# Optimization experiments

Hardware: AMD Instinct MI355X
Metric: run time of the kernel (lower is better)

Reference implementation:

```python
import jax, jax.numpy as jnp
from jax import lax
import numpy as np

INF = 1e10


def _fps_indices(xyz, npoint, start):
    """Farthest point sampling. xyz:(B,N,3), start:(B,) int32 -> (B,npoint) indices."""
    B, N, _ = xyz.shape

    def step(carry, _):
        distance, farthest = carry  # (B,N), (B,)
        # gather current centroid: (B,1,3)
        centroid = xyz[jnp.arange(B), farthest][:, None, :]
        dist = jnp.sum((xyz - centroid) ** 2, axis=-1)  # (B,N)
        distance = jnp.minimum(distance, dist)  # torch where(dist<distance, dist, distance)
        new_farthest = jnp.argmax(distance, axis=-1)
        return (distance, new_farthest), farthest

    init_dist = jnp.full((B, N), INF, dtype=xyz.dtype)
    (_, _), centroids = lax.scan(step, (init_dist, start), None, length=npoint)
    return centroids.T  # (B, npoint)


def setup_inputs() -> dict:
    key = jax.random.key(0)
    B, N = 16, 131072
    xyz = jax.random.normal(key, (B, N, 3), dtype=jnp.float32)
    return {"xyz": xyz, "npoint": 1024}


def reference(xyz, npoint):
    B, N, _ = xyz.shape
    # torch code picks a random starting index per batch; use a fixed jax PRNG
    start = jax.random.randint(jax.random.fold_in(jax.random.key(0), 1), (B,), 0, N)
    idx = _fps_indices(xyz, npoint, start)  # (B, npoint) int
    new_xyz = xyz[jnp.arange(B)[:, None], idx]  # (B, npoint, 3)
    return new_xyz, idx
```

## Files before the change

kernel.cpp:

```cpp
#include <hip/hip_runtime.h>
#include <stdint.h>

#define NB   16
#define WPB  16
#define NTHR 512
#define PPT  16

__device__ __forceinline__ void tf2x32(uint32_t k0, uint32_t k1,
                                       uint32_t x0, uint32_t x1,
                                       uint32_t &y0, uint32_t &y1) {
  uint32_t ks2 = k0 ^ k1 ^ 0x1BD11BDAu;
  uint32_t v0 = x0 + k0, v1 = x1 + k1;
#define TFR(r) { v0 += v1; v1 = (v1 << (r)) | (v1 >> (32 - (r))); v1 ^= v0; }
  TFR(13) TFR(15) TFR(26) TFR(6)   v0 += k1;  v1 += ks2 + 1u;
  TFR(17) TFR(29) TFR(16) TFR(24)  v0 += ks2; v1 += k0 + 2u;
  TFR(13) TFR(15) TFR(26) TFR(6)   v0 += k0;  v1 += k1 + 3u;
  TFR(17) TFR(29) TFR(16) TFR(24)  v0 += k1;  v1 += ks2 + 4u;
  TFR(13) TFR(15) TFR(26) TFR(6)   v0 += ks2; v1 += k0 + 5u;
#undef TFR
  y0 = v0; y1 = v1;
}

__global__ __launch_bounds__(NTHR, 4)
void FPSampler_42099269435595_kernel(const float* __restrict__ xyz,
                                     const int* __restrict__ npoint_ptr,
                                     float* __restrict__ out,
                                     unsigned long long* __restrict__ slots,
                                     int N) {
  const int blk  = blockIdx.x;
  const int b    = blk >> 4;
  const int w    = blk & (WPB - 1);
  const int tid  = threadIdx.x;
  const int wave = tid >> 6;
  const int lane = tid & 63;
  const int npoint = npoint_ptr[0];

  const float* __restrict__ xb = xyz + (size_t)b * N * 3;
  const int pts_per_wg = N / WPB;
  const int p0 = w * pts_per_wg + tid;

  float px[PPT], py[PPT], pz[PPT], dist[PPT];
#pragma unroll
  for (int k = 0; k < PPT; ++k) {
    size_t p = (size_t)(p0 + k * NTHR);
    px[k] = xb[3 * p + 0];
    py[k] = xb[3 * p + 1];
    pz[k] = xb[3 * p + 2];
    dist[k] = 1e10f;
  }

  uint32_t fk0, fk1, s0, s1, r0, r1;
  tf2x32(0u, 0u, 0u, 1u, fk0, fk1);
  tf2x32(fk0, fk1, 0u, 1u, s0, s1);
  tf2x32(s0, s1, 0u, (uint32_t)b, r0, r1);
  uint32_t far = (r0 ^ r1) & 0x1FFFFu;

  __shared__ unsigned long long lds_red[NTHR / 64];
  __shared__ unsigned long long lds_win;

  float* out_xyz = out;
  float* out_idx = out + (size_t)NB * npoint * 3;

  for (int i = 0; i < npoint; ++i) {
    float cx = xb[3 * (size_t)far + 0];
    float cy = xb[3 * (size_t)far + 1];
    float cz = xb[3 * (size_t)far + 2];
    if (w == 0 && tid == 0) {
      size_t o = (size_t)b * npoint + i;
      out_xyz[3 * o + 0] = cx;
      out_xyz[3 * o + 1] = cy;
      out_xyz[3 * o + 2] = cz;
      out_idx[o] = (float)far;
    }
    if (i == npoint - 1) break;

    float best = -1.0f;
    uint32_t bidx = 0;
#pragma unroll
    for (int k = 0; k < PPT; ++k) {
#pragma clang fp contract(off)
      float dx = px[k] - cx, dy = py[k] - cy, dz = pz[k] - cz;
      float d = (dx * dx + dy * dy) + dz * dz;
      float nd = fminf(dist[k], d);
      dist[k] = nd;
      if (nd > best) { best = nd; bidx = (uint32_t)(p0 + k * NTHR); }
    }

    unsigned long long pk =
        ((unsigned long long)(uint32_t)(i + 1) << 51) |
        ((unsigned long long)__float_as_uint(best) << 19) |
        (unsigned long long)(0x7FFFFu - bidx);

#pragma unroll
    for (int off = 32; off >= 1; off >>= 1) {
      unsigned long long o = __shfl_xor(pk, off);
      if (o > pk) pk = o;
    }
    if (lane == 0) lds_red[wave] = pk;
    __syncthreads();

    unsigned long long* myslot = &slots[((size_t)(i & 1) * NB + b) * WPB];
    if (tid == 0) {
      unsigned long long m = lds_red[0];
#pragma unroll
      for (int q = 1; q < NTHR / 64; ++q)
        if (lds_red[q] > m) m = lds_red[q];
      __hip_atomic_store(&myslot[w], m, __ATOMIC_RELAXED,
                         __HIP_MEMORY_SCOPE_AGENT);
    }
    if (wave == 0) {
      unsigned long long v = 0;
      if (lane < WPB) {
        const uint32_t tag = (uint32_t)(i + 1);
        do {
          v = __hip_atomic_load(&myslot[lane], __ATOMIC_RELAXED,
                                __HIP_MEMORY_SCOPE_AGENT);
        } while ((uint32_t)(v >> 51) != tag);
      }
#pragma unroll
      for (int off = 8; off >= 1; off >>= 1) {
        unsigned long long o = __shfl_xor(v, off);
        if (o > v) v = o;
      }
      if (lane == 0) lds_win = v;
    }
    __syncthreads();
    far = 0x7FFFFu - (uint32_t)(lds_win & 0x7FFFFu);
  }
}

extern "C" void kernel_launch(void* const* d_in, const int* in_sizes, int n_in,
                              void* d_out, int out_size, void* d_ws, size_t ws_size,
                              hipStream_t stream) {
  const float* xyz = (const float*)d_in[0];
  const int* npoint = (const int*)d_in[1];
  int N = in_sizes[0] / (NB * 3);

  hipMemsetAsync(d_ws, 0, (size_t)2 * NB * WPB * sizeof(unsigned long long),
                 stream);
  FPSampler_42099269435595_kernel<<<NB * WPB, NTHR, 0, stream>>>(
      xyz, npoint, (float*)d_out, (unsigned long long*)d_ws, N);
}
```

Baseline: 2.506 ms.

## Carry winner coordinates through cross-block exchange to avoid global centroid reload

Each thread tracks the coordinates of its best point, and each wave picks them out with ballot and shuffle. Every workgroup publishes its key plus x/y/z as four tagged 64-bit words in the slot array. Wave 0 of every block then polls all 64 words in parallel and takes the winning centroid directly, so the dependent global load of the next centroid at the start of each iteration goes away. The block-level reduction moves from a serial loop in one thread to a shuffle across wave 0. This costs more atomic stores and polling traffic per iteration and lowers the launch-bounds occupancy hint to 2.

```diff
diff --git a/kernel.cpp b/kernel.cpp
--- a/kernel.cpp
+++ b/kernel.cpp
@@ -1,10 +1,11 @@
 #include <hip/hip_runtime.h>
 #include <stdint.h>
 
-#define NB   16
-#define WPB  16
-#define NTHR 512
-#define PPT  16
+#define NB    16
+#define WPB   16
+#define NTHR  512
+#define NWAVE (NTHR / 64)
+#define PPT   16
 
 __device__ __forceinline__ void tf2x32(uint32_t k0, uint32_t k1,
                                        uint32_t x0, uint32_t x1,
@@ -21,7 +22,8 @@
   y0 = v0; y1 = v1;
 }
 
-__global__ __launch_bounds__(NTHR, 4)
+
+__global__ __launch_bounds__(NTHR, 2)
 void FPSampler_42099269435595_kernel(const float* __restrict__ xyz,
                                      const int* __restrict__ npoint_ptr,
                                      float* __restrict__ out,
@@ -36,8 +38,7 @@
   const int npoint = npoint_ptr[0];
 
   const float* __restrict__ xb = xyz + (size_t)b * N * 3;
-  const int pts_per_wg = N / WPB;
-  const int p0 = w * pts_per_wg + tid;
+  const int p0 = w * (N / WPB) + tid;
 
   float px[PPT], py[PPT], pz[PPT], dist[PPT];
 #pragma unroll
@@ -48,6 +49,10 @@
     pz[k] = xb[3 * p + 2];
     dist[k] = 1e10f;
   }
+#pragma unroll
+  for (int k = 0; k < PPT; ++k) {
+    asm volatile("" : "+v"(px[k]), "+v"(py[k]), "+v"(pz[k]));
+  }
 
   uint32_t fk0, fk1, s0, s1, r0, r1;
   tf2x32(0u, 0u, 0u, 1u, fk0, fk1);
@@ -55,16 +60,19 @@
   tf2x32(s0, s1, 0u, (uint32_t)b, r0, r1);
   uint32_t far = (r0 ^ r1) & 0x1FFFFu;
 
-  __shared__ unsigned long long lds_red[NTHR / 64];
-  __shared__ unsigned long long lds_win;
+  float cx = xb[3 * (size_t)far + 0];
+  float cy = xb[3 * (size_t)far + 1];
+  float cz = xb[3 * (size_t)far + 2];
+
+  __shared__ unsigned long long lds_key[NWAVE];
+  __shared__ float lds_x[NWAVE], lds_y[NWAVE], lds_z[NWAVE];
+  __shared__ unsigned int lds_bfar;
+  __shared__ float lds_bcx, lds_bcy, lds_bcz;
 
   float* out_xyz = out;
   float* out_idx = out + (size_t)NB * npoint * 3;
 
   for (int i = 0; i < npoint; ++i) {
-    float cx = xb[3 * (size_t)far + 0];
-    float cy = xb[3 * (size_t)far + 1];
-    float cz = xb[3 * (size_t)far + 2];
     if (w == 0 && tid == 0) {
       size_t o = (size_t)b * npoint + i;
       out_xyz[3 * o + 0] = cx;
@@ -74,7 +82,7 @@
     }
     if (i == npoint - 1) break;
 
-    float best = -1.0f;
+    float best = -1.0f, bx = 0.f, by = 0.f, bz = 0.f;
     uint32_t bidx = 0;
 #pragma unroll
     for (int k = 0; k < PPT; ++k) {
@@ -83,49 +91,92 @@
       float d = (dx * dx + dy * dy) + dz * dz;
       float nd = fminf(dist[k], d);
       dist[k] = nd;
-      if (nd > best) { best = nd; bidx = (uint32_t)(p0 + k * NTHR); }
+      if (nd > best) {
+        best = nd; bidx = (uint32_t)(p0 + k * NTHR);
+        bx = px[k]; by = py[k]; bz = pz[k];
+      }
     }
 
-    unsigned long long pk =
-        ((unsigned long long)(uint32_t)(i + 1) << 51) |
+    unsigned long long mykey =
         ((unsigned long long)__float_as_uint(best) << 19) |
         (unsigned long long)(0x7FFFFu - bidx);
-
+    unsigned long long pk = mykey;
 #pragma unroll
     for (int off = 32; off >= 1; off >>= 1) {
       unsigned long long o = __shfl_xor(pk, off);
       if (o > pk) pk = o;
     }
-    if (lane == 0) lds_red[wave] = pk;
+    unsigned long long bal = __ballot(mykey == pk);
+    int wl = __ffsll(bal) - 1;
+    float wx = __shfl(bx, wl), wy = __shfl(by, wl), wz = __shfl(bz, wl);
+    if (lane == 0) {
+      lds_key[wave] = pk;
+      lds_x[wave] = wx; lds_y[wave] = wy; lds_z[wave] = wz;
+    }
     __syncthreads();
 
-    unsigned long long* myslot = &slots[((size_t)(i & 1) * NB + b) * WPB];
-    if (tid == 0) {
-      unsigned long long m = lds_red[0];
+    unsigned long long* base =
+        slots + (size_t)(((i & 1) * NB + b)) * (WPB * 4);
+    const uint32_t tag = (uint32_t)(i + 1);
+
+    if (wave == 0) {
+      unsigned long long k8 = (lane < NWAVE) ? lds_key[lane] : 0ull;
+      unsigned long long m8 = k8;
 #pragma unroll
-      for (int q = 1; q < NTHR / 64; ++q)
-        if (lds_red[q] > m) m = lds_red[q];
-      __hip_atomic_store(&myslot[w], m, __ATOMIC_RELAXED,
-                         __HIP_MEMORY_SCOPE_AGENT);
-    }
-    if (wave == 0) {
-      unsigned long long v = 0;
-      if (lane < WPB) {
-        const uint32_t tag = (uint32_t)(i + 1);
-        do {
-          v = __hip_atomic_load(&myslot[lane], __ATOMIC_RELAXED,
-                                __HIP_MEMORY_SCOPE_AGENT);
-        } while ((uint32_t)(v >> 51) != tag);
+      for (int off = 4; off >= 1; off >>= 1) {
+        unsigned long long o = __shfl_xor(m8, off);
+        if (o > m8) m8 = o;
       }
+      unsigned long long bal8 = __ballot(lane < NWAVE && k8 == m8);
+      int wv = __ffsll(bal8) - 1;
+      if (lane == 0) {
+        unsigned long long* myslot = base + w * 4;
+        unsigned long long word0 = ((unsigned long long)tag << 51) | m8;
+        unsigned long long w1 =
+            ((unsigned long long)__float_as_uint(lds_x[wv]) << 32) | tag;
+        unsigned long long w2 =
+            ((unsigned long long)__float_as_uint(lds_y[wv]) << 32) | tag;
+        unsigned long long w3 =
+            ((unsigned long long)__float_as_uint(lds_z[wv]) << 32) | tag;
+        __hip_atomic_store(&myslot[0], word0, __ATOMIC_RELAXED,
+                           __HIP_MEMORY_SCOPE_AGENT);
+        __hip_atomic_store(&myslot[1], w1, __ATOMIC_RELAXED,
+                           __HIP_MEMORY_SCOPE_AGENT);
+        __hip_atomic_store(&myslot[2], w2, __ATOMIC_RELAXED,
+                           __HIP_MEMORY_SCOPE_AGENT);
+        __hip_atomic_store(&myslot[3], w3, __ATOMIC_RELAXED,
+                           __HIP_MEMORY_SCOPE_AGENT);
+      }
+
+      unsigned long long v;
+      uint32_t t;
+      do {
+        v = __hip_atomic_load(base + lane, __ATOMIC_RELAXED,
+                              __HIP_MEMORY_SCOPE_AGENT);
+        t = (lane & 3) ? (uint32_t)v : (uint32_t)(v >> 51);
+      } while (__any(t != tag));
+
+      unsigned long long key = __shfl(v, (lane & 15) << 2);
+      unsigned long long gk = key;
 #pragma unroll
       for (int off = 8; off >= 1; off >>= 1) {
-        unsigned long long o = __shfl_xor(v, off);
-        if (o > v) v = o;
+        unsigned long long o = __shfl_xor(gk, off);
+        if (o > gk) gk = o;
       }
-      if (lane == 0) lds_win = v;
+      unsigned long long gbal = __ballot(key == gk);
+      int ws = (__ffsll(gbal) - 1) & 15;
+      uint32_t nfar = 0x7FFFFu - (uint32_t)(gk & 0x7FFFFu);
+      float ncx = __uint_as_float((uint32_t)(__shfl(v, (ws << 2) | 1) >> 32));
+      float ncy = __uint_as_float((uint32_t)(__shfl(v, (ws << 2) | 2) >> 32));
+      float ncz = __uint_as_float((uint32_t)(__shfl(v, (ws << 2) | 3) >> 32));
+      if (lane == 0) {
+        lds_bfar = nfar;
+        lds_bcx = ncx; lds_bcy = ncy; lds_bcz = ncz;
+      }
     }
     __syncthreads();
-    far = 0x7FFFFu - (uint32_t)(lds_win & 0x7FFFFu);
+    far = lds_bfar;
+    cx = lds_bcx; cy = lds_bcy; cz = lds_bcz;
   }
 }
 
@@ -136,7 +187,8 @@
   const int* npoint = (const int*)d_in[1];
   int N = in_sizes[0] / (NB * 3);
 
-  hipMemsetAsync(d_ws, 0, (size_t)2 * NB * WPB * sizeof(unsigned long long),
+  hipMemsetAsync(d_ws, 0,
+                 (size_t)2 * NB * WPB * 4 * sizeof(unsigned long long),
                  stream);
   FPSampler_42099269435595_kernel<<<NB * WPB, NTHR, 0, stream>>>(
       xyz, npoint, (float*)d_out, (unsigned long long*)d_ws, N);
```

New measurement: 2.906 ms. 16.0% more time.

## Replace block barriers with per-wave global slot reduction and move points to LDS

Applied to the files above, without the earlier changes.

Each wave now publishes its own argmax candidate to a global slot array (WPB*NWAVE slots per batch), and every wave independently polls all 128 slots and reduces them. This removes both __syncthreads per iteration and the single-thread serial combine. Point coordinates move from registers to volatile LDS to free VGPRs, and the next centroid is loaded through a scalar index. The cost is more global polling traffic per iteration and extra LDS reads in the inner loop.

```diff
diff --git a/kernel.cpp b/kernel.cpp
--- a/kernel.cpp
+++ b/kernel.cpp
@@ -1,10 +1,13 @@
 #include <hip/hip_runtime.h>
 #include <stdint.h>
 
-#define NB   16
-#define WPB  16
-#define NTHR 512
-#define PPT  16
+#define NB    16
+#define WPB   16
+#define NTHR  512
+#define NWAVE 8
+#define PPT   16
+#define SLOTS_PER_BATCH (WPB * NWAVE)
+#define LDS_BYTES (3 * PPT * NTHR * 4)
 
 __device__ __forceinline__ void tf2x32(uint32_t k0, uint32_t k1,
                                        uint32_t x0, uint32_t x1,
@@ -27,6 +30,8 @@
                                      float* __restrict__ out,
                                      unsigned long long* __restrict__ slots,
                                      int N) {
+#pragma clang fp contract(off)
+  extern __shared__ float smem[];
   const int blk  = blockIdx.x;
   const int b    = blk >> 4;
   const int w    = blk & (WPB - 1);
@@ -36,16 +41,19 @@
   const int npoint = npoint_ptr[0];
 
   const float* __restrict__ xb = xyz + (size_t)b * N * 3;
-  const int pts_per_wg = N / WPB;
-  const int p0 = w * pts_per_wg + tid;
+  const int p0 = w * (N / WPB) + tid;
 
-  float px[PPT], py[PPT], pz[PPT], dist[PPT];
+  volatile float* lx = smem;
+  volatile float* ly = smem + PPT * NTHR;
+  volatile float* lz = smem + 2 * PPT * NTHR;
+
+  float dist[PPT];
 #pragma unroll
   for (int k = 0; k < PPT; ++k) {
     size_t p = (size_t)(p0 + k * NTHR);
-    px[k] = xb[3 * p + 0];
-    py[k] = xb[3 * p + 1];
-    pz[k] = xb[3 * p + 2];
+    lx[k * NTHR + tid] = xb[3 * p + 0];
+    ly[k * NTHR + tid] = xb[3 * p + 1];
+    lz[k * NTHR + tid] = xb[3 * p + 2];
     dist[k] = 1e10f;
   }
 
@@ -55,17 +63,16 @@
   tf2x32(s0, s1, 0u, (uint32_t)b, r0, r1);
   uint32_t far = (r0 ^ r1) & 0x1FFFFu;
 
-  __shared__ unsigned long long lds_red[NTHR / 64];
-  __shared__ unsigned long long lds_win;
+  int sfar = __builtin_amdgcn_readfirstlane((int)far);
+  float cx = xb[3 * (size_t)sfar + 0];
+  float cy = xb[3 * (size_t)sfar + 1];
+  float cz = xb[3 * (size_t)sfar + 2];
 
   float* out_xyz = out;
   float* out_idx = out + (size_t)NB * npoint * 3;
 
   for (int i = 0; i < npoint; ++i) {
-    float cx = xb[3 * (size_t)far + 0];
-    float cy = xb[3 * (size_t)far + 1];
-    float cz = xb[3 * (size_t)far + 2];
-    if (w == 0 && tid == 0) {
+    if (w == 0 && tid == NTHR - 1) {
       size_t o = (size_t)b * npoint + i;
       out_xyz[3 * o + 0] = cx;
       out_xyz[3 * o + 1] = cy;
@@ -78,54 +85,52 @@
     uint32_t bidx = 0;
 #pragma unroll
     for (int k = 0; k < PPT; ++k) {
-#pragma clang fp contract(off)
-      float dx = px[k] - cx, dy = py[k] - cy, dz = pz[k] - cz;
+      float xk = lx[k * NTHR + tid];
+      float yk = ly[k * NTHR + tid];
+      float zk = lz[k * NTHR + tid];
+      float dx = xk - cx, dy = yk - cy, dz = zk - cz;
       float d = (dx * dx + dy * dy) + dz * dz;
       float nd = fminf(dist[k], d);
       dist[k] = nd;
       if (nd > best) { best = nd; bidx = (uint32_t)(p0 + k * NTHR); }
     }
 
+    const uint32_t tag = (uint32_t)(i + 1);
     unsigned long long pk =
-        ((unsigned long long)(uint32_t)(i + 1) << 51) |
+        ((unsigned long long)tag << 51) |
         ((unsigned long long)__float_as_uint(best) << 19) |
         (unsigned long long)(0x7FFFFu - bidx);
-
 #pragma unroll
     for (int off = 32; off >= 1; off >>= 1) {
       unsigned long long o = __shfl_xor(pk, off);
       if (o > pk) pk = o;
     }
-    if (lane == 0) lds_red[wave] = pk;
-    __syncthreads();
+    unsigned long long* base =
+        slots + (size_t)((i & 1) * NB + b) * SLOTS_PER_BATCH;
+    if (lane == 0)
+      __hip_atomic_store(base + w * NWAVE + wave, pk, __ATOMIC_RELAXED,
+                         __HIP_MEMORY_SCOPE_AGENT);
 
-    unsigned long long* myslot = &slots[((size_t)(i & 1) * NB + b) * WPB];
-    if (tid == 0) {
-      unsigned long long m = lds_red[0];
+    unsigned long long v0, v1;
+    do {
+      v0 = __hip_atomic_load(base + lane, __ATOMIC_RELAXED,
+                             __HIP_MEMORY_SCOPE_AGENT);
+      v1 = __hip_atomic_load(base + 64 + lane, __ATOMIC_RELAXED,
+                             __HIP_MEMORY_SCOPE_AGENT);
+    } while (__any(((uint32_t)(v0 >> 51) != tag) |
+                   ((uint32_t)(v1 >> 51) != tag)));
+
+    unsigned long long gk = (v0 > v1) ? v0 : v1;
 #pragma unroll
-      for (int q = 1; q < NTHR / 64; ++q)
-        if (lds_red[q] > m) m = lds_red[q];
-      __hip_atomic_store(&myslot[w], m, __ATOMIC_RELAXED,
-                         __HIP_MEMORY_SCOPE_AGENT);
+    for (int off = 32; off >= 1; off >>= 1) {
+      unsigned long long o = __shfl_xor(gk, off);
+      if (o > gk) gk = o;
     }
-    if (wave == 0) {
-      unsigned long long v = 0;
-      if (lane < WPB) {
-        const uint32_t tag = (uint32_t)(i + 1);
-        do {
-          v = __hip_atomic_load(&myslot[lane], __ATOMIC_RELAXED,
-                                __HIP_MEMORY_SCOPE_AGENT);
-        } while ((uint32_t)(v >> 51) != tag);
-      }
-#pragma unroll
-      for (int off = 8; off >= 1; off >>= 1) {
-        unsigned long long o = __shfl_xor(v, off);
-        if (o > v) v = o;
-      }
-      if (lane == 0) lds_win = v;
-    }
-    __syncthreads();
-    far = 0x7FFFFu - (uint32_t)(lds_win & 0x7FFFFu);
+    far = 0x7FFFFu - (uint32_t)(gk & 0x7FFFFu);
+    sfar = __builtin_amdgcn_readfirstlane((int)far);
+    cx = xb[3 * (size_t)sfar + 0];
+    cy = xb[3 * (size_t)sfar + 1];
+    cz = xb[3 * (size_t)sfar + 2];
   }
 }
 
@@ -136,8 +141,12 @@
   const int* npoint = (const int*)d_in[1];
   int N = in_sizes[0] / (NB * 3);
 
-  hipMemsetAsync(d_ws, 0, (size_t)2 * NB * WPB * sizeof(unsigned long long),
+  hipFuncSetAttribute((const void*)FPSampler_42099269435595_kernel,
+                      hipFuncAttributeMaxDynamicSharedMemorySize, LDS_BYTES);
+
+  hipMemsetAsync(d_ws, 0,
+                 (size_t)2 * NB * SLOTS_PER_BATCH * sizeof(unsigned long long),
                  stream);
-  FPSampler_42099269435595_kernel<<<NB * WPB, NTHR, 0, stream>>>(
+  FPSampler_42099269435595_kernel<<<NB * WPB, NTHR, LDS_BYTES, stream>>>(
       xyz, npoint, (float*)d_out, (unsigned long long*)d_ws, N);
 }
```

Result: slower. 7.139 ms (+184.9%).
